# Optimization experiments

Measured on AMD Instinct MI355X. Metric: run time of the kernel, lower is better.

The kernel has to match this reference:

```python
import jax, jax.numpy as jnp
import numpy as np

B, T, D = 1, 2048, 1024
HQ, HKV, HD = 16, 4, 64
G = HQ // HKV
E, TOPK, F = 8, 2, 2752
LB = 0.01
SCALE = HD ** -0.5


def setup_inputs() -> dict:
    key = jax.random.key(0)
    ks = jax.random.split(key, 12)
    s = 0.02
    return {
        "x": jax.random.normal(ks[0], (B, T, D), jnp.float32),
        "g1": jnp.ones((D,), jnp.float32),
        "g2": jnp.ones((D,), jnp.float32),
        "wq": jax.random.normal(ks[1], (D, HQ * HD), jnp.float32) * s,
        "wk": jax.random.normal(ks[2], (D, HKV * HD), jnp.float32) * s,
        "wv": jax.random.normal(ks[3], (D, HKV * HD), jnp.float32) * s,
        "wo": jax.random.normal(ks[4], (D, D), jnp.float32) * s,
        "gate_w": jax.random.normal(ks[5], (D, E), jnp.float32) * s,
        "we_gate": jax.random.normal(ks[6], (E, D, F), jnp.float32) * s,
        "we_up": jax.random.normal(ks[7], (E, D, F), jnp.float32) * s,
        "we_down": jax.random.normal(ks[8], (E, F, D), jnp.float32) * s,
    }


def _rmsnorm(x, g, eps=1e-6):
    return x * g * jax.lax.rsqrt(jnp.mean(x * x, axis=-1, keepdims=True) + eps)


def _rope(q, k):
    # q: [B,HQ,T,HD], k: [B,HKV,T,HD]; standard rotate-half RoPE
    pos = jnp.arange(T, dtype=jnp.float32)
    inv_freq = 1.0 / (10000.0 ** (jnp.arange(0, HD, 2, dtype=jnp.float32) / HD))
    ang = pos[:, None] * inv_freq[None, :]                  # [T, HD/2]
    cos = jnp.concatenate([jnp.cos(ang), jnp.cos(ang)], -1)  # [T, HD]
    sin = jnp.concatenate([jnp.sin(ang), jnp.sin(ang)], -1)

    def rot_half(x):
        x1, x2 = jnp.split(x, 2, axis=-1)
        return jnp.concatenate([-x2, x1], axis=-1)

    def apply(x):
        return x * cos + rot_half(x) * sin
    return apply(q), apply(k)


def _attention(x, g1, wq, wk, wv, wo):
    h = _rmsnorm(x, g1)
    q = (h @ wq).reshape(B, T, HQ, HD).transpose(0, 2, 1, 3)   # [B,HQ,T,HD]
    k = (h @ wk).reshape(B, T, HKV, HD).transpose(0, 2, 1, 3)  # [B,HKV,T,HD]
    v = (h @ wv).reshape(B, T, HKV, HD).transpose(0, 2, 1, 3)
    q, k = _rope(q, k)
    qg = q.reshape(B, HKV, G, T, HD)
    # grouped scores without materializing repeated K/V
    scores = jnp.einsum('bkgtd,bksd->bkgts', qg, k) * SCALE     # [B,HKV,G,T,T]
    causal = jnp.tril(jnp.ones((T, T), bool))
    scores = jnp.where(causal, scores, jnp.float32(-jnp.inf))
    w = jax.nn.softmax(scores, axis=-1)
    o = jnp.einsum('bkgts,bksd->bkgtd', w, v)                  # [B,HKV,G,T,HD]
    o = o.reshape(B, HQ, T, HD).transpose(0, 2, 1, 3).reshape(B, T, D)
    return o @ wo


def _moe(x, g2, gate_w, we_gate, we_up, we_down):
    h = _rmsnorm(x, g2).reshape(B * T, D)                      # [N,D]
    N = B * T
    logits = h @ gate_w                                        # [N,E]
    probs = jax.nn.softmax(logits, axis=-1)
    topv, topi = jax.lax.top_k(probs, TOPK)                    # [N,TOPK]
    topv = topv / (topv.sum(-1, keepdims=True) + 1e-8)
    # dense combine weights [N,E]: same math as masked per-expert dispatch
    combine = jnp.zeros((N, E), h.dtype).at[jnp.arange(N)[:, None], topi].add(topv)
    gh = jnp.einsum('nd,edf->enf', h, we_gate)
    up = jnp.einsum('nd,edf->enf', h, we_up)
    y = jnp.einsum('enf,efd->end', jax.nn.silu(gh) * up, we_down)
    out = jnp.einsum('end,ne->nd', y, combine).reshape(B, T, D)
    # load-balancing aux loss
    frac = jnp.zeros((E,), probs.dtype).at[topi.reshape(-1)].add(1.0) / (N * TOPK)
    load = probs.mean(axis=0)
    aux = LB * E * jnp.sum(frac * load)
    return out, aux


def reference(x, g1, g2, wq, wk, wv, wo, gate_w, we_gate, we_up, we_down):
    x = x + _attention(x, g1, wq, wk, wv, wo)
    moe_out, aux = _moe(x, g2, gate_w, we_gate, we_up, we_down)
    x = x + moe_out
    return x, aux
```

## Files before the change

kernel.cpp:

```cpp
#include <hip/hip_runtime.h>
#include <cstdint>

typedef __attribute__((ext_vector_type(8))) short short8;
typedef __attribute__((ext_vector_type(4))) float floatx4;
typedef __attribute__((ext_vector_type(4))) unsigned short ushort4v;
typedef unsigned short ushort;

#define T_LEN 2048
#define D_DIM 1024
#define HQn 16
#define HKVn 4
#define NE 8
#define FF 2752
#define NTOK 2048
#define NSLOT 4096
#define ATT_SCALE 0.125f
#define GATE_TPB 16

#define WAITCNT(N) asm volatile("s_waitcnt vmcnt(" #N ")" ::: "memory")

__device__ inline ushort f2bf(float f) {
  union { float f; unsigned int i; } v; v.f = f;
  unsigned int r = v.i + 0x7fffu + ((v.i >> 16) & 1u);
  return (ushort)(r >> 16);
}
__device__ inline float bf2f(ushort h) {
  union { unsigned int i; float f; } v; v.i = ((unsigned int)h) << 16;
  return v.f;
}
__device__ inline void split8(const float* v, short8& hi, short8& lo) {
#pragma unroll
  for (int i = 0; i < 8; i++) {
    ushort h = f2bf(v[i]);
    hi[i] = (short)h;
    lo[i] = (short)f2bf(v[i] - bf2f(h));
  }
}
__device__ inline floatx4 mfma16(short8 a, short8 b, floatx4 c) {
  return __builtin_amdgcn_mfma_f32_16x16x32_bf16(a, b, c, 0, 0, 0);
}
#define DMA16(g, l)                                                              \
  __builtin_amdgcn_global_load_lds((const __attribute__((address_space(1))) void*)(g), \
                                   (__attribute__((address_space(3))) void*)(l), 16, 0, 0)

__global__ __launch_bounds__(256) void k_cvtT(const float* __restrict__ src,
                                              ushort* __restrict__ dst, int R, int C) {
  __shared__ float tile[32][33];
  size_t sb = (size_t)blockIdx.z * R * C;
  const float* s = src + sb;
  ushort* d = dst + sb;
  int r0 = blockIdx.y * 32, c0 = blockIdx.x * 32;
  int tc = threadIdx.x & 31, tr = threadIdx.x >> 5;
#pragma unroll
  for (int i = 0; i < 4; i++)
    tile[tr + i * 8][tc] = s[(size_t)(r0 + tr + i * 8) * C + c0 + tc];
  __syncthreads();
#pragma unroll
  for (int i = 0; i < 4; i++) {
    int cc = tr + i * 8;
    d[(size_t)(c0 + cc) * R + r0 + tc] = f2bf(tile[tc][cc]);
  }
}

__global__ __launch_bounds__(256) void k_cvtT2(const float* __restrict__ src,
                                               ushort* __restrict__ dh,
                                               ushort* __restrict__ dl, int R, int C) {
  __shared__ float tile[32][33];
  int r0 = blockIdx.y * 32, c0 = blockIdx.x * 32;
  int tc = threadIdx.x & 31, tr = threadIdx.x >> 5;
#pragma unroll
  for (int i = 0; i < 4; i++)
    tile[tr + i * 8][tc] = src[(size_t)(r0 + tr + i * 8) * C + c0 + tc];
  __syncthreads();
#pragma unroll
  for (int i = 0; i < 4; i++) {
    int cc = tr + i * 8;
    float v = tile[tc][cc];
    ushort h = f2bf(v);
    dh[(size_t)(c0 + cc) * R + r0 + tc] = h;
    dl[(size_t)(c0 + cc) * R + r0 + tc] = f2bf(v - bf2f(h));
  }
}

__global__ __launch_bounds__(256) void k_rmsnorm2(const float* __restrict__ x,
                                                  const float* __restrict__ g,
                                                  ushort* __restrict__ oh,
                                                  ushort* __restrict__ ol) {
  int row = blockIdx.x;
  int t = threadIdx.x;
  const float4* x4 = (const float4*)(x + (size_t)row * D_DIM);
  float4 v = x4[t];
  float ss = v.x * v.x + v.y * v.y + v.z * v.z + v.w * v.w;
#pragma unroll
  for (int off = 32; off; off >>= 1) ss += __shfl_xor(ss, off, 64);
  __shared__ float red[4];
  if ((t & 63) == 0) red[t >> 6] = ss;
  __syncthreads();
  float tot = red[0] + red[1] + red[2] + red[3];
  float sc = rsqrtf(tot * (1.0f / D_DIM) + 1e-6f);
  const float4* g4 = (const float4*)g;
  float4 gv = g4[t];
  float vals[4] = {v.x * gv.x * sc, v.y * gv.y * sc, v.z * gv.z * sc, v.w * gv.w * sc};
  ushort4v h4, l4;
#pragma unroll
  for (int i = 0; i < 4; i++) {
    ushort h = f2bf(vals[i]);
    h4[i] = h;
    l4[i] = f2bf(vals[i] - bf2f(h));
  }
  *(ushort4v*)(oh + (size_t)row * D_DIM + t * 4) = h4;
  *(ushort4v*)(ol + (size_t)row * D_DIM + t * 4) = l4;
}

__global__ __launch_bounds__(256) void k_sgemm(const ushort* __restrict__ Ahg,
                                               const ushort* __restrict__ Alg,
                                               const ushort* __restrict__ Bhg,
                                               const ushort* __restrict__ Blg,
                                               float* __restrict__ C,
                                               const float* __restrict__ res,
                                               int N, int K) {
  __shared__ __align__(16) ushort L[36864];
  int tid = threadIdx.x;
  int m0 = blockIdx.y * 64, n0 = blockIdx.x * 128;
  int wave = tid >> 6, lane = tid & 63, quad = lane >> 4, l15 = lane & 15;
  int wm = (wave >> 1) * 32, wn = (wave & 1) * 64;
  floatx4 acc[2][4];
#pragma unroll
  for (int i = 0; i < 2; i++)
#pragma unroll
    for (int j = 0; j < 4; j++) acc[i][j] = (floatx4){0.f, 0.f, 0.f, 0.f};
  const ushort* src[6];
  int off[6];
  int srow = lane >> 2;
  int kc = ((lane & 3) ^ ((lane >> 3) & 3)) * 8;
#pragma unroll
  for (int j = 0; j < 6; j++) {
    int c = wave * 6 + j;
    if (c < 4) {
      src[j] = Ahg + (size_t)(m0 + c * 16 + srow) * K + kc;
      off[j] = c * 512;
    } else if (c < 8) {
      src[j] = Alg + (size_t)(m0 + (c - 4) * 16 + srow) * K + kc;
      off[j] = 2048 + (c - 4) * 512;
    } else if (c < 16) {
      src[j] = Bhg + (size_t)(n0 + (c - 8) * 16 + srow) * K + kc;
      off[j] = 4096 + (c - 8) * 512;
    } else {
      src[j] = Blg + (size_t)(n0 + (c - 16) * 16 + srow) * K + kc;
      off[j] = 8192 + (c - 16) * 512;
    }
  }
  auto stage = [&](ushort* Ld, int k0) {
#pragma unroll
    for (int j = 0; j < 6; j++) DMA16(src[j] + k0, Ld + off[j]);
  };
  auto compute = [&](const ushort* Ld) {
    const ushort* Ah = Ld;
    const ushort* Al = Ld + 2048;
    const ushort* Bh = Ld + 4096;
    const ushort* Bl = Ld + 8192;
    short8 ah[2], al[2], bh[4], bl[4];
#pragma unroll
    for (int mt = 0; mt < 2; mt++) {
      int ar = wm + mt * 16 + l15;
      int sw = (quad ^ ((ar >> 1) & 3)) * 8;
      ah[mt] = *(short8*)&Ah[ar * 32 + sw];
      al[mt] = *(short8*)&Al[ar * 32 + sw];
    }
#pragma unroll
    for (int nt = 0; nt < 4; nt++) {
      int br = wn + nt * 16 + l15;
      int sw = (quad ^ ((br >> 1) & 3)) * 8;
      bh[nt] = *(short8*)&Bh[br * 32 + sw];
      bl[nt] = *(short8*)&Bl[br * 32 + sw];
    }
#pragma unroll
    for (int mt = 0; mt < 2; mt++)
#pragma unroll
      for (int nt = 0; nt < 4; nt++) {
        acc[mt][nt] = mfma16(ah[mt], bh[nt], acc[mt][nt]);
        acc[mt][nt] = mfma16(ah[mt], bl[nt], acc[mt][nt]);
        acc[mt][nt] = mfma16(al[mt], bh[nt], acc[mt][nt]);
      }
  };
  int ntile = K >> 5;
  stage(L, 0);
  stage(L + 12288, 32);
  int cb = 0;
  for (int t = 0; t < ntile; t++) {
    if (t + 1 < ntile) { WAITCNT(6); } else { WAITCNT(0); }
    __builtin_amdgcn_s_barrier();
    __builtin_amdgcn_sched_barrier(0);
    if (t + 2 < ntile) {
      int sb = cb + 2; if (sb >= 3) sb -= 3;
      stage(L + sb * 12288, (t + 2) << 5);
    }
    compute(L + cb * 12288);
    if (++cb == 3) cb = 0;
  }
#pragma unroll
  for (int mt = 0; mt < 2; mt++) {
    int row = m0 + wm + mt * 16 + quad * 4;
#pragma unroll
    for (int nt2 = 0; nt2 < 4; nt2++) {
      int col = n0 + wn + nt2 * 16 + l15;
#pragma unroll
      for (int r = 0; r < 4; r++) {
        float v = acc[mt][nt2][r];
        if (res) v += res[(size_t)(row + r) * N + col];
        C[(size_t)(row + r) * N + col] = v;
      }
    }
  }
}

__global__ __launch_bounds__(256) void k_rope_cvt(const float* __restrict__ qkvf,
                                                  ushort* __restrict__ qhi,
                                                  ushort* __restrict__ qlo,
                                                  ushort* __restrict__ khi,
                                                  ushort* __restrict__ klo) {
  int t = blockIdx.x;
  const float* row = qkvf + (size_t)t * 1536;
  for (int it = threadIdx.x; it < (HQn + HKVn) * 32; it += 256) {
    int hh = it >> 5, i = it & 31;
    float inv = powf(10000.0f, -(float)i / 32.0f);
    float ang = (float)t * inv;
    float c = cosf(ang), s = sinf(ang);
    const float* p;
    ushort *dh, *dl;
    size_t base;
    if (hh < HQn) {
      p = row + hh * 64;
      base = ((size_t)hh * T_LEN + t) * 64;
      dh = qhi; dl = qlo;
    } else {
      int h2 = hh - HQn;
      p = row + 1024 + h2 * 64;
      base = ((size_t)h2 * T_LEN + t) * 64;
      dh = khi; dl = klo;
    }
    float a = p[i], b = p[i + 32];
    float v0 = a * c - b * s;
    float v1 = b * c + a * s;
    ushort h0 = f2bf(v0);
    dh[base + i] = h0;
    dl[base + i] = f2bf(v0 - bf2f(h0));
    ushort h1 = f2bf(v1);
    dh[base + i + 32] = h1;
    dl[base + i + 32] = f2bf(v1 - bf2f(h1));
  }
}

__global__ __launch_bounds__(256) void k_vT(const float* __restrict__ qkvf,
                                            ushort* __restrict__ vbth,
                                            ushort* __restrict__ vbtl) {
  __shared__ float tile[32][33];
  int t0 = blockIdx.x * 32;
  int dh = blockIdx.y;
  int col0 = 1280 + dh * 32;
  int tc = threadIdx.x & 31, tr = threadIdx.x >> 5;
#pragma unroll
  for (int i = 0; i < 4; i++)
    tile[tr + i * 8][tc] = qkvf[(size_t)(t0 + tr + i * 8) * 1536 + col0 + tc];
  __syncthreads();
#pragma unroll
  for (int i = 0; i < 4; i++) {
    int dd = tr + i * 8;
    float v = tile[tc][dd];
    ushort h = f2bf(v);
    size_t idx = (size_t)(dh * 32 + dd) * T_LEN + t0 + tc;
    vbth[idx] = h;
    vbtl[idx] = f2bf(v - bf2f(h));
  }
}

__global__ __launch_bounds__(256) void k_attn(const ushort* __restrict__ qhi,
                                              const ushort* __restrict__ qlo,
                                              const ushort* __restrict__ khi,
                                              const ushort* __restrict__ klo,
                                              const ushort* __restrict__ vbth,
                                              const ushort* __restrict__ vbtl,
                                              ushort* __restrict__ obh,
                                              ushort* __restrict__ obl) {
  __shared__ __align__(16) ushort Kh[4096], Kl[4096], Vh[4096], Vl[4096];
  __shared__ ushort Psh[4 * 16 * 72], Psl[4 * 16 * 72];
  int qh = blockIdx.y, kvh = qh >> 2;
  int tid = threadIdx.x, wave = tid >> 6, lane = tid & 63;
  int quad = lane >> 4, l15 = lane & 15;
  int sx = l15 >> 1;
  int rlb = lane >> 3;
  int csb = (lane & 7) ^ (lane >> 4);
#pragma unroll 1
  for (int hf = 0; hf < 2; hf++) {
    int xt = hf ? (31 - (int)blockIdx.x) : (int)blockIdx.x;
    int r0 = xt * 64;
    const ushort* qbh_ = qhi + ((size_t)qh * T_LEN + r0 + wave * 16 + l15) * 64;
    const ushort* qbl_ = qlo + ((size_t)qh * T_LEN + r0 + wave * 16 + l15) * 64;
    short8 aqh0 = *(const short8*)&qbh_[quad * 8];
    short8 aqh1 = *(const short8*)&qbh_[32 + quad * 8];
    short8 aql0 = *(const short8*)&qbl_[quad * 8];
    short8 aql1 = *(const short8*)&qbl_[32 + quad * 8];
    floatx4 oacc[4];
#pragma unroll
    for (int nt = 0; nt < 4; nt++) oacc[nt] = (floatx4){0.f, 0.f, 0.f, 0.f};
    float mrun[4], lrun[4];
#pragma unroll
    for (int r = 0; r < 4; r++) { mrun[r] = -INFINITY; lrun[r] = 0.f; }
    for (int cc = 0; cc <= xt; cc++) {
      __syncthreads();
      if (wave < 2) {
        const ushort* G = (wave == 0) ? khi : klo;
        ushort* L = (wave == 0) ? Kh : Kl;
        size_t rbase = (size_t)kvh * T_LEN + cc * 64;
#pragma unroll
        for (int i = 0; i < 8; i++) {
          int ch = csb ^ ((i & 1) * 4);
          DMA16(G + (rbase + i * 8 + rlb) * 64 + ch * 8, L + i * 512);
        }
      } else {
        const ushort* G = (wave == 2) ? vbth : vbtl;
        ushort* L = (wave == 2) ? Vh : Vl;
#pragma unroll
        for (int i = 0; i < 8; i++) {
          int ch = csb ^ ((i & 1) * 4);
          DMA16(G + ((size_t)(kvh * 64 + i * 8 + rlb)) * T_LEN + cc * 64 + ch * 8,
                L + i * 512);
        }
      }
      __syncthreads();
      floatx4 s[4];
#pragma unroll
      for (int nt = 0; nt < 4; nt++) {
        int row = nt * 16 + l15;
        short8 bh0 = *(short8*)&Kh[row * 64 + (quad ^ sx) * 8];
        short8 bh1 = *(short8*)&Kh[row * 64 + ((4 + quad) ^ sx) * 8];
        short8 bl0 = *(short8*)&Kl[row * 64 + (quad ^ sx) * 8];
        short8 bl1 = *(short8*)&Kl[row * 64 + ((4 + quad) ^ sx) * 8];
        floatx4 z = (floatx4){0.f, 0.f, 0.f, 0.f};
        z = mfma16(aqh0, bh0, z);
        z = mfma16(aqh1, bh1, z);
        z = mfma16(aqh0, bl0, z);
        z = mfma16(aqh1, bl1, z);
        z = mfma16(aql0, bh0, z);
        z = mfma16(aql1, bh1, z);
        s[nt] = z;
      }
      int rowg0 = r0 + wave * 16 + quad * 4;
#pragma unroll
      for (int nt = 0; nt < 4; nt++) {
        int colg = cc * 64 + nt * 16 + l15;
#pragma unroll
        for (int r = 0; r < 4; r++) {
          float v = s[nt][r] * ATT_SCALE;
          s[nt][r] = (colg > rowg0 + r) ? -INFINITY : v;
        }
      }
      float mnew[4], alpha[4], psum[4];
#pragma unroll
      for (int r = 0; r < 4; r++) {
        float mx = fmaxf(fmaxf(s[0][r], s[1][r]), fmaxf(s[2][r], s[3][r]));
#pragma unroll
        for (int off = 1; off < 16; off <<= 1) mx = fmaxf(mx, __shfl_xor(mx, off, 64));
        mnew[r] = fmaxf(mrun[r], mx);
        psum[r] = 0.f;
      }
#pragma unroll
      for (int nt = 0; nt < 4; nt++)
#pragma unroll
        for (int r = 0; r < 4; r++) {
          float p = __expf(s[nt][r] - mnew[r]);
          s[nt][r] = p;
          psum[r] += p;
        }
#pragma unroll
      for (int r = 0; r < 4; r++) {
        float ps = psum[r];
#pragma unroll
        for (int off = 1; off < 16; off <<= 1) ps += __shfl_xor(ps, off, 64);
        alpha[r] = __expf(mrun[r] - mnew[r]);
        lrun[r] = lrun[r] * alpha[r] + ps;
        mrun[r] = mnew[r];
      }
#pragma unroll
      for (int nt = 0; nt < 4; nt++)
#pragma unroll
        for (int r = 0; r < 4; r++) oacc[nt][r] *= alpha[r];
#pragma unroll
      for (int nt = 0; nt < 4; nt++)
#pragma unroll
        for (int r = 0; r < 4; r++) {
          float p = s[nt][r];
          ushort ph = f2bf(p);
          Psh[wave * 1152 + (quad * 4 + r) * 72 + nt * 16 + l15] = ph;
          Psl[wave * 1152 + (quad * 4 + r) * 72 + nt * 16 + l15] = f2bf(p - bf2f(ph));
        }
      short8 aph0 = *(short8*)&Psh[wave * 1152 + l15 * 72 + quad * 8];
      short8 aph1 = *(short8*)&Psh[wave * 1152 + l15 * 72 + 32 + quad * 8];
      short8 apl0 = *(short8*)&Psl[wave * 1152 + l15 * 72 + quad * 8];
      short8 apl1 = *(short8*)&Psl[wave * 1152 + l15 * 72 + 32 + quad * 8];
#pragma unroll
      for (int nt = 0; nt < 4; nt++) {
        int row = nt * 16 + l15;
        short8 bvh0 = *(short8*)&Vh[row * 64 + (quad ^ sx) * 8];
        short8 bvh1 = *(short8*)&Vh[row * 64 + ((4 + quad) ^ sx) * 8];
        short8 bvl0 = *(short8*)&Vl[row * 64 + (quad ^ sx) * 8];
        short8 bvl1 = *(short8*)&Vl[row * 64 + ((4 + quad) ^ sx) * 8];
        oacc[nt] = mfma16(aph0, bvh0, oacc[nt]);
        oacc[nt] = mfma16(aph1, bvh1, oacc[nt]);
        oacc[nt] = mfma16(aph0, bvl0, oacc[nt]);
        oacc[nt] = mfma16(aph1, bvl1, oacc[nt]);
        oacc[nt] = mfma16(apl0, bvh0, oacc[nt]);
        oacc[nt] = mfma16(apl1, bvh1, oacc[nt]);
      }
    }
#pragma unroll
    for (int nt = 0; nt < 4; nt++)
#pragma unroll
      for (int r = 0; r < 4; r++) {
        int rowg = r0 + wave * 16 + quad * 4 + r;
        float v = oacc[nt][r] / lrun[r];
        ushort h = f2bf(v);
        size_t idx = (size_t)rowg * D_DIM + qh * 64 + nt * 16 + l15;
        obh[idx] = h;
        obl[idx] = f2bf(v - bf2f(h));
      }
  }
}

__global__ __launch_bounds__(256) void k_gate(const float* __restrict__ x1,
                                              const float* __restrict__ g2,
                                              const float* __restrict__ gw,
                                              int* __restrict__ counts,
                                              int* __restrict__ ids,
                                              float* __restrict__ wts,
                                              float* __restrict__ load_sum) {
  __shared__ float lsum[NE];
  __shared__ int lcount[NE];
  __shared__ int lbase[NE];
  __shared__ int ltok[GATE_TPB * 2];
  __shared__ int lexp[GATE_TPB * 2];
  __shared__ float lwt[GATE_TPB * 2];
  int tid = threadIdx.x, wave = tid >> 6, lane = tid & 63;
  if (tid < NE) { lsum[tid] = 0.f; lcount[tid] = 0; }
  __syncthreads();
  int t0 = blockIdx.x * GATE_TPB;
#pragma unroll
  for (int tt = 0; tt < GATE_TPB / 4; tt++) {
    int tloc = tt * 4 + wave;
    int token = t0 + tloc;
    const float* xp = x1 + (size_t)token * D_DIM;
    float acc[NE] = {};
    float ss = 0.f;
    for (int d = lane; d < D_DIM; d += 64) {
      float xv = xp[d];
      ss += xv * xv;
      float hv = xv * g2[d];
#pragma unroll
      for (int e = 0; e < NE; e++) acc[e] += hv * gw[d * NE + e];
    }
#pragma unroll
    for (int off = 32; off; off >>= 1) ss += __shfl_xor(ss, off, 64);
#pragma unroll
    for (int e = 0; e < NE; e++)
#pragma unroll
      for (int off = 32; off; off >>= 1) acc[e] += __shfl_xor(acc[e], off, 64);
    if (lane == 0) {
      float sc = rsqrtf(ss * (1.0f / D_DIM) + 1e-6f);
      float mx = -1e30f;
#pragma unroll
      for (int e = 0; e < NE; e++) { acc[e] *= sc; mx = fmaxf(mx, acc[e]); }
      float p[NE], sum = 0.f;
#pragma unroll
      for (int e = 0; e < NE; e++) { p[e] = expf(acc[e] - mx); sum += p[e]; }
#pragma unroll
      for (int e = 0; e < NE; e++) p[e] /= sum;
      int i1 = 0;
#pragma unroll
      for (int e = 1; e < NE; e++) if (acc[e] > acc[i1]) i1 = e;
      int i2 = (i1 == 0) ? 1 : 0;
#pragma unroll
      for (int e = 0; e < NE; e++) if (e != i1 && acc[e] > acc[i2]) i2 = e;
      float denom = p[i1] + p[i2] + 1e-8f;
      int slot = tloc * 2;
      lexp[slot] = i1; ltok[slot] = token; lwt[slot] = p[i1] / denom;
      lexp[slot + 1] = i2; ltok[slot + 1] = token; lwt[slot + 1] = p[i2] / denom;
      atomicAdd(&lcount[i1], 1);
      atomicAdd(&lcount[i2], 1);
#pragma unroll
      for (int e = 0; e < NE; e++) atomicAdd(&lsum[e], p[e]);
    }
  }
  __syncthreads();
  if (tid < NE) {
    lbase[tid] = atomicAdd(&counts[tid], lcount[tid]);
    atomicAdd(&load_sum[tid], lsum[tid]);
    lcount[tid] = 0;
  }
  __syncthreads();
  if (tid < GATE_TPB * 2) {
    int e = lexp[tid];
    int off = atomicAdd(&lcount[e], 1);
    int pos = lbase[e] + off;
    ids[e * NTOK + pos] = ltok[tid];
    wts[e * NTOK + pos] = lwt[tid];
  }
}

__global__ void k_offsets(const int* __restrict__ counts, int* __restrict__ offsets) {
  if (threadIdx.x == 0 && blockIdx.x == 0) {
    int s = 0;
    for (int e = 0; e < NE; e++) { offsets[e] = s; s += counts[e]; }
  }
}

__global__ __launch_bounds__(256) void k_moe_gateup(const ushort* __restrict__ h,
                                                    const ushort* __restrict__ wgT,
                                                    const ushort* __restrict__ wuT,
                                                    const int* __restrict__ ids,
                                                    const float* __restrict__ wts,
                                                    const int* __restrict__ counts,
                                                    const int* __restrict__ offsets,
                                                    ushort* __restrict__ act) {
  int e = blockIdx.z;
  int cnt = counts[e];
  int m0 = blockIdx.y * 128;
  if (m0 >= cnt) return;
  int n0 = blockIdx.x * 64;
  __shared__ __align__(16) ushort L[24576];
  __shared__ int toks[128];
  __shared__ float wrow[128];
  int tid = threadIdx.x;
  if (tid < 128) {
    int mm = m0 + tid;
    toks[tid] = (mm < cnt) ? ids[e * NTOK + mm] : 0;
    wrow[tid] = (mm < cnt) ? wts[e * NTOK + mm] : 0.f;
  }
  __syncthreads();
  int wave = tid >> 6, lane = tid & 63, quad = lane >> 4, l15 = lane & 15;
  int wm = (wave >> 1) * 64, wn = (wave & 1) * 32;
  const ushort* Wg = wgT + (size_t)e * FF * D_DIM;
  const ushort* Wu = wuT + (size_t)e * FF * D_DIM;
  const ushort* src[4];
  int off[4];
  int srow = lane >> 2;
  int kc = ((lane & 3) ^ ((lane >> 3) & 3)) * 8;
#pragma unroll
  for (int j = 0; j < 4; j++) {
    int c = wave * 4 + j;
    if (c < 8) {
      src[j] = h + (size_t)toks[c * 16 + srow] * D_DIM + kc;
      off[j] = c * 512;
    } else if (c < 12) {
      src[j] = Wg + (size_t)(n0 + (c - 8) * 16 + srow) * D_DIM + kc;
      off[j] = 4096 + (c - 8) * 512;
    } else {
      src[j] = Wu + (size_t)(n0 + (c - 12) * 16 + srow) * D_DIM + kc;
      off[j] = 6144 + (c - 12) * 512;
    }
  }
  floatx4 accg[4][2], accu[4][2];
#pragma unroll
  for (int i = 0; i < 4; i++)
#pragma unroll
    for (int j = 0; j < 2; j++) {
      accg[i][j] = (floatx4){0.f, 0.f, 0.f, 0.f};
      accu[i][j] = (floatx4){0.f, 0.f, 0.f, 0.f};
    }
  auto stage = [&](ushort* Ld, int k0) {
#pragma unroll
    for (int j = 0; j < 4; j++) DMA16(src[j] + k0, Ld + off[j]);
  };
  auto compute = [&](const ushort* Ld) {
    const ushort* As = Ld;
    const ushort* Bg = Ld + 4096;
    const ushort* Bu = Ld + 6144;
    short8 aF[4], bgF[2], buF[2];
#pragma unroll
    for (int mt = 0; mt < 4; mt++) {
      int ar = wm + mt * 16 + l15;
      int sw = (quad ^ ((ar >> 1) & 3)) * 8;
      aF[mt] = *(short8*)&As[ar * 32 + sw];
    }
#pragma unroll
    for (int nt = 0; nt < 2; nt++) {
      int br = wn + nt * 16 + l15;
      int sw = (quad ^ ((br >> 1) & 3)) * 8;
      bgF[nt] = *(short8*)&Bg[br * 32 + sw];
      buF[nt] = *(short8*)&Bu[br * 32 + sw];
    }
#pragma unroll
    for (int mt = 0; mt < 4; mt++)
#pragma unroll
      for (int nt = 0; nt < 2; nt++) {
        accg[mt][nt] = mfma16(aF[mt], bgF[nt], accg[mt][nt]);
        accu[mt][nt] = mfma16(aF[mt], buF[nt], accu[mt][nt]);
      }
  };
  stage(L, 0);
  stage(L + 8192, 32);
  int cb = 0;
  for (int t = 0; t < 32; t++) {
    if (t + 1 < 32) { WAITCNT(4); } else { WAITCNT(0); }
    __builtin_amdgcn_s_barrier();
    __builtin_amdgcn_sched_barrier(0);
    if (t + 2 < 32) {
      int sb = cb + 2; if (sb >= 3) sb -= 3;
      stage(L + sb * 8192, (t + 2) << 5);
    }
    compute(L + cb * 8192);
    if (++cb == 3) cb = 0;
  }
  int aoff = offsets[e];
#pragma unroll
  for (int mt = 0; mt < 4; mt++) {
    int mrow = wm + mt * 16 + quad * 4;
#pragma unroll
    for (int nt = 0; nt < 2; nt++) {
      int col = n0 + wn + nt * 16 + l15;
#pragma unroll
      for (int r = 0; r < 4; r++) {
        int ml = mrow + r;
        if (m0 + ml < cnt) {
          float g = accg[mt][nt][r];
          float u = accu[mt][nt][r];
          float sil = g / (1.f + __expf(-g));
          act[(size_t)(aoff + m0 + ml) * FF + col] = f2bf(sil * u * wrow[ml]);
        }
      }
    }
  }
}

__global__ __launch_bounds__(256) void k_moe_down(const ushort* __restrict__ act,
                                                  const ushort* __restrict__ wdT,
                                                  const int* __restrict__ ids,
                                                  const int* __restrict__ counts,
                                                  const int* __restrict__ offsets,
                                                  float* __restrict__ moe_acc) {
  int e = blockIdx.z & 7;
  int kh = blockIdx.z >> 3;
  int cnt = counts[e];
  int m0 = blockIdx.y * 128;
  if (m0 >= cnt) return;
  int n0 = blockIdx.x * 128;
  __shared__ __align__(16) ushort L[24576];
  __shared__ int toks[128];
  int tid = threadIdx.x;
  if (tid < 128) {
    int mm = m0 + tid;
    toks[tid] = (mm < cnt) ? ids[e * NTOK + mm] : 0;
  }
  __syncthreads();
  int wave = tid >> 6, lane = tid & 63, quad = lane >> 4, l15 = lane & 15;
  int wm = (wave >> 1) * 64, wn = (wave & 1) * 64;
  int aoff = offsets[e];
  const ushort* Wd = wdT + (size_t)e * D_DIM * FF;
  const ushort* src[4];
  int off[4];
  int srow = lane >> 2;
  int kc = ((lane & 3) ^ ((lane >> 3) & 3)) * 8;
#pragma unroll
  for (int j = 0; j < 4; j++) {
    int c = wave * 4 + j;
    if (c < 8) {
      src[j] = act + (size_t)(aoff + m0 + c * 16 + srow) * FF + kc;
      off[j] = c * 512;
    } else {
      src[j] = Wd + (size_t)(n0 + (c - 8) * 16 + srow) * FF + kc;
      off[j] = 4096 + (c - 8) * 512;
    }
  }
  floatx4 acc[4][4];
#pragma unroll
  for (int i = 0; i < 4; i++)
#pragma unroll
    for (int j = 0; j < 4; j++) acc[i][j] = (floatx4){0.f, 0.f, 0.f, 0.f};
  auto stage = [&](ushort* Ld, int k0) {
#pragma unroll
    for (int j = 0; j < 4; j++) DMA16(src[j] + k0, Ld + off[j]);
  };
  auto compute = [&](const ushort* Ld) {
    const ushort* As = Ld;
    const ushort* Bs = Ld + 4096;
    short8 aF[4], bF[4];
#pragma unroll
    for (int mt = 0; mt < 4; mt++) {
      int ar = wm + mt * 16 + l15;
      int sw = (quad ^ ((ar >> 1) & 3)) * 8;
      aF[mt] = *(short8*)&As[ar * 32 + sw];
    }
#pragma unroll
    for (int nt = 0; nt < 4; nt++) {
      int br = wn + nt * 16 + l15;
      int sw = (quad ^ ((br >> 1) & 3)) * 8;
      bF[nt] = *(short8*)&Bs[br * 32 + sw];
    }
#pragma unroll
    for (int mt = 0; mt < 4; mt++)
#pragma unroll
      for (int nt = 0; nt < 4; nt++) acc[mt][nt] = mfma16(aF[mt], bF[nt], acc[mt][nt]);
  };
  int kbeg = kh * 1376;
  stage(L, kbeg);
  stage(L + 8192, kbeg + 32);
  int cb = 0;
  for (int t = 0; t < 43; t++) {
    if (t + 1 < 43) { WAITCNT(4); } else { WAITCNT(0); }
    __builtin_amdgcn_s_barrier();
    __builtin_amdgcn_sched_barrier(0);
    if (t + 2 < 43) {
      int sb = cb + 2; if (sb >= 3) sb -= 3;
      stage(L + sb * 8192, kbeg + ((t + 2) << 5));
    }
    compute(L + cb * 8192);
    if (++cb == 3) cb = 0;
  }
#pragma unroll
  for (int mt = 0; mt < 4; mt++) {
    int mrow = wm + mt * 16 + quad * 4;
#pragma unroll
    for (int nt2 = 0; nt2 < 4; nt2++) {
      int col = n0 + wn + nt2 * 16 + l15;
#pragma unroll
      for (int r = 0; r < 4; r++) {
        int ml = mrow + r;
        if (m0 + ml < cnt)
          atomicAdd(&moe_acc[(size_t)toks[ml] * D_DIM + col], acc[mt][nt2][r]);
      }
    }
  }
}

__global__ __launch_bounds__(256) void k_add(const float* __restrict__ a,
                                             const float* __restrict__ b,
                                             float* __restrict__ o) {
  int i = blockIdx.x * 256 + threadIdx.x;
  float4 va = ((const float4*)a)[i];
  float4 vb = ((const float4*)b)[i];
  float4 vo;
  vo.x = va.x + vb.x; vo.y = va.y + vb.y; vo.z = va.z + vb.z; vo.w = va.w + vb.w;
  ((float4*)o)[i] = vo;
}

__global__ void k_aux(const int* __restrict__ counts, const float* __restrict__ load_sum,
                      float* __restrict__ out_aux) {
  if (threadIdx.x == 0 && blockIdx.x == 0) {
    float s = 0.f;
    for (int e = 0; e < NE; e++)
      s += ((float)counts[e] / (float)NSLOT) * (load_sum[e] / (float)NTOK);
    *out_aux = 0.01f * (float)NE * s;
  }
}

extern "C" void kernel_launch(void* const* d_in, const int* in_sizes, int n_in,
                              void* d_out, int out_size, void* d_ws, size_t ws_size,
                              hipStream_t stream) {
  const float* x = (const float*)d_in[0];
  const float* g1 = (const float*)d_in[1];
  const float* g2 = (const float*)d_in[2];
  const float* wq = (const float*)d_in[3];
  const float* wk = (const float*)d_in[4];
  const float* wv = (const float*)d_in[5];
  const float* wo = (const float*)d_in[6];
  const float* gate_w = (const float*)d_in[7];
  const float* we_gate = (const float*)d_in[8];
  const float* we_up = (const float*)d_in[9];
  const float* we_down = (const float*)d_in[10];
  float* out = (float*)d_out;

  char* w = (char*)d_ws;
  size_t o = 0;
  auto alloc = [&](size_t bytes) -> char* {
    char* p = w + o;
    o = (o + bytes + 255) & ~(size_t)255;
    return p;
  };
  ushort* h1h = (ushort*)alloc((size_t)NTOK * D_DIM * 2);
  ushort* h1l = (ushort*)alloc((size_t)NTOK * D_DIM * 2);
  float* qkvf = (float*)alloc((size_t)NTOK * 1536 * 4);
  ushort* qhi = (ushort*)alloc((size_t)HQn * T_LEN * 64 * 2);
  ushort* qlo = (ushort*)alloc((size_t)HQn * T_LEN * 64 * 2);
  ushort* khi = (ushort*)alloc((size_t)HKVn * T_LEN * 64 * 2);
  ushort* klo = (ushort*)alloc((size_t)HKVn * T_LEN * 64 * 2);
  ushort* vbth = (ushort*)alloc((size_t)HKVn * 64 * T_LEN * 2);
  ushort* vbtl = (ushort*)alloc((size_t)HKVn * 64 * T_LEN * 2);
  ushort* obh = (ushort*)alloc((size_t)NTOK * D_DIM * 2);
  ushort* obl = (ushort*)alloc((size_t)NTOK * D_DIM * 2);
  float* x1 = (float*)alloc((size_t)NTOK * D_DIM * 4);
  float* moe_acc = (float*)alloc((size_t)NTOK * D_DIM * 4);
  ushort* act = (ushort*)alloc((size_t)(NSLOT + 128) * FF * 2);
  ushort* qkvwTh = (ushort*)alloc((size_t)1536 * 1024 * 2);
  ushort* qkvwTl = (ushort*)alloc((size_t)1536 * 1024 * 2);
  ushort* woTh = (ushort*)alloc((size_t)1024 * 1024 * 2);
  ushort* woTl = (ushort*)alloc((size_t)1024 * 1024 * 2);
  ushort* h2h = (ushort*)alloc((size_t)NTOK * D_DIM * 2);
  ushort* h2l = (ushort*)alloc((size_t)NTOK * D_DIM * 2);
  ushort* wgT = (ushort*)alloc((size_t)NE * FF * D_DIM * 2);
  ushort* wuT = (ushort*)alloc((size_t)NE * FF * D_DIM * 2);
  ushort* wdT = (ushort*)alloc((size_t)NE * D_DIM * FF * 2);
  int* counts = (int*)alloc(NE * 4);
  int* offsets = (int*)alloc(NE * 4);
  float* load_sum = (float*)alloc(NE * 4);
  int* ids = (int*)alloc((size_t)NE * NTOK * 4);
  float* wts = (float*)alloc((size_t)NE * NTOK * 4);

  hipMemsetAsync(moe_acc, 0, (size_t)NTOK * D_DIM * 4, stream);
  hipMemsetAsync(counts, 0, 768, stream);

  k_cvtT2<<<dim3(32, 32), 256, 0, stream>>>(wq, qkvwTh, qkvwTl, 1024, 1024);
  k_cvtT2<<<dim3(8, 32), 256, 0, stream>>>(wk, qkvwTh + (size_t)1024 * 1024,
                                           qkvwTl + (size_t)1024 * 1024, 1024, 256);
  k_cvtT2<<<dim3(8, 32), 256, 0, stream>>>(wv, qkvwTh + (size_t)1280 * 1024,
                                           qkvwTl + (size_t)1280 * 1024, 1024, 256);
  k_cvtT2<<<dim3(32, 32), 256, 0, stream>>>(wo, woTh, woTl, 1024, 1024);
  k_cvtT<<<dim3(86, 32, 8), 256, 0, stream>>>(we_gate, wgT, 1024, 2752);
  k_cvtT<<<dim3(86, 32, 8), 256, 0, stream>>>(we_up, wuT, 1024, 2752);
  k_cvtT<<<dim3(32, 86, 8), 256, 0, stream>>>(we_down, wdT, 2752, 1024);

  k_rmsnorm2<<<NTOK, 256, 0, stream>>>(x, g1, h1h, h1l);
  k_sgemm<<<dim3(12, 32), 256, 0, stream>>>(h1h, h1l, qkvwTh, qkvwTl, qkvf, nullptr,
                                            1536, 1024);
  k_rope_cvt<<<T_LEN, 256, 0, stream>>>(qkvf, qhi, qlo, khi, klo);
  k_vT<<<dim3(64, 8), 256, 0, stream>>>(qkvf, vbth, vbtl);
  k_attn<<<dim3(16, 16), 256, 0, stream>>>(qhi, qlo, khi, klo, vbth, vbtl, obh, obl);
  k_sgemm<<<dim3(8, 32), 256, 0, stream>>>(obh, obl, woTh, woTl, x1, x, 1024, 1024);

  k_rmsnorm2<<<NTOK, 256, 0, stream>>>(x1, g2, h2h, h2l);
  k_gate<<<NTOK / GATE_TPB, 256, 0, stream>>>(x1, g2, gate_w, counts, ids, wts, load_sum);
  k_offsets<<<1, 1, 0, stream>>>(counts, offsets);
  k_moe_gateup<<<dim3(43, 16, 8), 256, 0, stream>>>(h2h, wgT, wuT, ids, wts, counts,
                                                    offsets, act);
  k_moe_down<<<dim3(8, 16, 16), 256, 0, stream>>>(act, wdT, ids, counts, offsets, moe_acc);
  k_add<<<(NTOK * D_DIM) / (256 * 4), 256, 0, stream>>>(x1, moe_acc, out);
  k_aux<<<1, 1, 0, stream>>>(counts, load_sum, out + (size_t)NTOK * D_DIM);
}
```

Before: 683.3 us.

## Remap MoE grids to 1D with XCD-aware swizzle, double-buffer gate/up LDS

Both MoE GEMM kernels now launch on a flat 1D grid and decode expert, M-tile and N-tile from the block index. Groups of eight consecutive blocks share the same M-tile across different N/expert tiles, which is meant to improve L2 reuse across the MI355X's chiplets. The gate/up kernel also replaces its three-stage waitcnt-based LDS pipeline with a simpler two-buffer scheme and a full __syncthreads per iteration. That lowers LDS use and may raise occupancy, but it risks less overlap between loads and MFMA compute.

```diff
diff --git a/kernel.cpp b/kernel.cpp
--- a/kernel.cpp
+++ b/kernel.cpp
@@ -521,12 +521,17 @@
                                                     const int* __restrict__ counts,
                                                     const int* __restrict__ offsets,
                                                     ushort* __restrict__ act) {
-  int e = blockIdx.z;
+  int p = blockIdx.x;
+  int k8 = p & 7, q = p >> 3;
+  int G = (q >> 4) * 8 + k8;
+  int m = q & 15;
+  int e = G / 43;
+  int n = G - e * 43;
   int cnt = counts[e];
-  int m0 = blockIdx.y * 128;
+  int m0 = m * 128;
   if (m0 >= cnt) return;
-  int n0 = blockIdx.x * 64;
-  __shared__ __align__(16) ushort L[24576];
+  int n0 = n * 64;
+  __shared__ __align__(16) ushort L0[8192], L1[8192];
   __shared__ int toks[128];
   __shared__ float wrow[128];
   int tid = threadIdx.x;
@@ -596,19 +601,17 @@
         accu[mt][nt] = mfma16(aF[mt], buF[nt], accu[mt][nt]);
       }
   };
-  stage(L, 0);
-  stage(L + 8192, 32);
-  int cb = 0;
+  stage(L0, 0);
+  __syncthreads();
   for (int t = 0; t < 32; t++) {
-    if (t + 1 < 32) { WAITCNT(4); } else { WAITCNT(0); }
-    __builtin_amdgcn_s_barrier();
-    __builtin_amdgcn_sched_barrier(0);
-    if (t + 2 < 32) {
-      int sb = cb + 2; if (sb >= 3) sb -= 3;
-      stage(L + sb * 8192, (t + 2) << 5);
-    }
-    compute(L + cb * 8192);
-    if (++cb == 3) cb = 0;
+    if ((t & 1) == 0) {
+      if (t + 1 < 32) stage(L1, (t + 1) << 5);
+      compute(L0);
+    } else {
+      if (t + 1 < 32) stage(L0, (t + 1) << 5);
+      compute(L1);
+    }
+    __syncthreads();
   }
   int aoff = offsets[e];
 #pragma unroll
@@ -637,12 +640,17 @@
                                                   const int* __restrict__ counts,
                                                   const int* __restrict__ offsets,
                                                   float* __restrict__ moe_acc) {
-  int e = blockIdx.z & 7;
-  int kh = blockIdx.z >> 3;
+  int p = blockIdx.x;
+  int k8 = p & 7, q = p >> 3;
+  int G = (q >> 4) * 8 + k8;
+  int m = q & 15;
+  int z = G >> 3;
+  int n = G & 7;
+  int e = z & 7, kh = z >> 3;
   int cnt = counts[e];
-  int m0 = blockIdx.y * 128;
+  int m0 = m * 128;
   if (m0 >= cnt) return;
-  int n0 = blockIdx.x * 128;
+  int n0 = n * 128;
   __shared__ __align__(16) ushort L[24576];
   __shared__ int toks[128];
   int tid = threadIdx.x;
@@ -828,9 +836,8 @@
   k_rmsnorm2<<<NTOK, 256, 0, stream>>>(x1, g2, h2h, h2l);
   k_gate<<<NTOK / GATE_TPB, 256, 0, stream>>>(x1, g2, gate_w, counts, ids, wts, load_sum);
   k_offsets<<<1, 1, 0, stream>>>(counts, offsets);
-  k_moe_gateup<<<dim3(43, 16, 8), 256, 0, stream>>>(h2h, wgT, wuT, ids, wts, counts,
-                                                    offsets, act);
-  k_moe_down<<<dim3(8, 16, 16), 256, 0, stream>>>(act, wdT, ids, counts, offsets, moe_acc);
+  k_moe_gateup<<<5504, 256, 0, stream>>>(h2h, wgT, wuT, ids, wts, counts, offsets, act);
+  k_moe_down<<<2048, 256, 0, stream>>>(act, wdT, ids, counts, offsets, moe_acc);
   k_add<<<(NTOK * D_DIM) / (256 * 4), 256, 0, stream>>>(x1, moe_acc, out);
   k_aux<<<1, 1, 0, stream>>>(counts, load_sum, out + (size_t)NTOK * D_DIM);
 }
```

After: 675.7 us. Within noise of the previous version (-1.1%).
